# Kernel optimization log

Measured on AMD Instinct MI355X. Metric: run time of the kernel, lower is better.

## Reference

```python
import jax, jax.numpy as jnp
import numpy as np

EMBED_DIM = 1024
NUM_HEADS = 16
HEAD_DIM = EMBED_DIM // NUM_HEADS  # 64
SCALING = 0.125
T, B = 2048, 2


def setup_inputs() -> dict:
    key = jax.random.key(0)
    k_q, k_len, k_w1, k_b1, k_w2, k_b2 = jax.random.split(key, 6)
    query = jax.random.normal(k_q, (T, B, EMBED_DIM), dtype=jnp.float32)
    # realistic padding: each sequence has a valid length in [T//2, T)
    lengths = jax.random.randint(k_len, (B,), T // 2, T)
    key_padding_mask = jnp.arange(T)[None, :] >= lengths[:, None]  # [B, T] bool, True = pad
    s1 = 1.0 / np.sqrt(EMBED_DIM)
    W_in = jax.random.uniform(k_w1, (3 * EMBED_DIM, EMBED_DIM), jnp.float32, -s1, s1)
    b_in = jax.random.uniform(k_b1, (3 * EMBED_DIM,), jnp.float32, -s1, s1)
    W_out = jax.random.uniform(k_w2, (EMBED_DIM, EMBED_DIM), jnp.float32, -s1, s1)
    b_out = jax.random.uniform(k_b2, (EMBED_DIM,), jnp.float32, -s1, s1)
    return {"query": query, "key_padding_mask": key_padding_mask,
            "W_in": W_in, "b_in": b_in, "W_out": W_out, "b_out": b_out}


def reference(query, key_padding_mask, W_in, b_in, W_out, b_out):
    # query: [T, B, E]; key_padding_mask: [B, S] bool (True = padded key)
    t, b, e = query.shape
    h, hd = NUM_HEADS, HEAD_DIM
    proj = query @ W_in.T + b_in                      # [T, B, 3E]
    q, k, v = jnp.split(proj, 3, axis=-1)             # each [T, B, E]
    q = q * SCALING

    def to_bh(x):  # [T, B, E] -> [B*H, T, hd], matching torch view+transpose
        return x.reshape(t, b * h, hd).transpose(1, 0, 2)

    q, k, v = to_bh(q), to_bh(k), to_bh(v)
    attn_weights = jnp.einsum('bth,bsh->bts', q, k)   # [B*H, T, S]
    attn_weights = attn_weights.reshape(b, h, t, t)
    attn_weights = jnp.where(key_padding_mask[:, None, None, :], -jnp.inf, attn_weights)
    # softmax computed in float32 then cast back, as in the original
    attn_weights = jax.nn.softmax(attn_weights.astype(jnp.float32), axis=-1).astype(query.dtype)
    # dropout p=0 (eval/inference) -> identity
    attn = jnp.einsum('bhts,bhsd->bhtd', attn_weights, v.reshape(b, h, t, hd))  # [B,H,T,hd]
    attn = attn.reshape(b * h, t, hd).transpose(1, 0, 2).reshape(t, b, e)       # [T,B,E]
    return attn @ W_out.T + b_out
```

## Files before the change

### kernel.cpp

```cpp
#include <hip/hip_runtime.h>
#include <hip/hip_bf16.h>
#include <stdint.h>
#include <stddef.h>

typedef __hip_bfloat16 bf16;
typedef __attribute__((ext_vector_type(4))) float f32x4;
typedef __attribute__((ext_vector_type(8))) short s16x8;
typedef __attribute__((ext_vector_type(4))) short s16x4;

#define AS1 __attribute__((address_space(1)))
#define AS3 __attribute__((address_space(3)))

__device__ __forceinline__ void async_ld16(const void* g, void* l) {
  __builtin_amdgcn_global_load_lds((AS1 void*)g, (AS3 void*)l, 16, 0, 0);
}

#if __has_builtin(__builtin_amdgcn_exp2f)
#define EXP2F(x) __builtin_amdgcn_exp2f(x)
#else
#define EXP2F(x) exp2f(x)
#endif

__device__ __forceinline__ unsigned pk_bf16(float a, float b) {
  unsigned ua = __builtin_bit_cast(unsigned, a);
  unsigned ub = __builtin_bit_cast(unsigned, b);
  ua += 0x7FFFu + ((ua >> 16) & 1u);
  ub += 0x7FFFu + ((ub >> 16) & 1u);
  return (ua >> 16) | (ub & 0xFFFF0000u);
}

__device__ __forceinline__ unsigned pk_trunc(float a, float b) {
  return __builtin_amdgcn_perm(__builtin_bit_cast(unsigned, b),
                               __builtin_bit_cast(unsigned, a), 0x07060302u);
}

__global__ __launch_bounds__(256) void convert_all_kernel(const float* __restrict__ q_src,
                                                          const float* __restrict__ wi_src,
                                                          const float* __restrict__ wo_src,
                                                          bf16* __restrict__ q_dst,
                                                          bf16* __restrict__ wi_dst,
                                                          bf16* __restrict__ wo_dst,
                                                          const void* __restrict__ mask,
                                                          int* __restrict__ lengths) {
  int blk = blockIdx.x;
  if (blk >= 4096) {
    __shared__ int s_any;
    __shared__ int s_cnt[256];
    const int tid = threadIdx.x;
    const int b = blk - 4096;
    const unsigned char* m8 = (const unsigned char*)mask;
    if (tid == 0) s_any = 0;
    __syncthreads();
    int local = 0;
    for (int i = tid; i < 4096; i += 256) local |= m8[i];
    if (local) atomicOr(&s_any, 1);
    __syncthreads();
    int cnt = 0;
    if (s_any) {
      for (int t = tid; t < 2048; t += 256) cnt += (m8[b * 2048 + t] == 0) ? 1 : 0;
    } else {
      const int* m32 = (const int*)mask;
      for (int t = tid; t < 2048; t += 256) cnt += (m32[b * 2048 + t] == 0) ? 1 : 0;
    }
    s_cnt[tid] = cnt;
    __syncthreads();
    for (int s = 128; s > 0; s >>= 1) {
      if (tid < s) s_cnt[tid] += s_cnt[tid + s];
      __syncthreads();
    }
    if (tid == 0) lengths[b] = s_cnt[0];
    return;
  }
  const float* src;
  bf16* dst;
  int base;
  if (blk < 2048)      { src = q_src;  dst = q_dst;  base = blk * 2048; }
  else if (blk < 3584) { src = wi_src; dst = wi_dst; base = (blk - 2048) * 2048; }
  else                 { src = wo_src; dst = wo_dst; base = (blk - 3584) * 2048; }
  int i = base + threadIdx.x * 8;
  float4 a = *(const float4*)(src + i);
  float4 b = *(const float4*)(src + i + 4);
  unsigned u[4];
  u[0] = pk_bf16(a.x, a.y); u[1] = pk_bf16(a.z, a.w);
  u[2] = pk_bf16(b.x, b.y); u[3] = pk_bf16(b.z, b.w);
  *(uint4*)(dst + i) = *(const uint4*)u;
}

__device__ __forceinline__ void gemm_mainloop(const bf16* __restrict__ A,
                                              const bf16* __restrict__ Bm,
                                              bf16* As, bf16* Bs,
                                              int m0, int n0, f32x4 (&acc)[4][4]) {
  const int K = 1024;
  const int tid = threadIdx.x;
  const int wave = tid >> 6, lane = tid & 63;
  const int col = lane & 15, quad = lane >> 4;
  const int wm = wave & 1, wn = wave >> 1;
#pragma unroll
  for (int mi = 0; mi < 4; mi++)
#pragma unroll
    for (int ni = 0; ni < 4; ni++) acc[mi][ni] = (f32x4){0.f, 0.f, 0.f, 0.f};

  const int c0 = wave * 128 + lane;
  const int rowA0 = c0 >> 2, kc0 = (c0 & 3) * 8;
  const int c1 = c0 + 64;
  const int rowA1 = c1 >> 2, kc1 = (c1 & 3) * 8;
  char* ldsA0 = (char*)As + (size_t)(wave * 128) * 16;
  char* ldsA1 = ldsA0 + 64 * 16;
  char* ldsB0 = (char*)Bs + (size_t)(wave * 128) * 16;
  char* ldsB1 = ldsB0 + 64 * 16;
  const bf16* gA0 = A + (size_t)(m0 + rowA0) * K + kc0;
  const bf16* gA1 = A + (size_t)(m0 + rowA1) * K + kc1;
  const bf16* gB0 = Bm + (size_t)(n0 + rowA0) * K + kc0;
  const bf16* gB1 = Bm + (size_t)(n0 + rowA1) * K + kc1;

  for (int k0 = 0; k0 < K; k0 += 32) {
    async_ld16(gA0 + k0, ldsA0);
    async_ld16(gA1 + k0, ldsA1);
    async_ld16(gB0 + k0, ldsB0);
    async_ld16(gB1 + k0, ldsB1);
    __syncthreads();
    s16x8 af[4], bfr[4];
#pragma unroll
    for (int mi = 0; mi < 4; mi++)
      af[mi] = *(const s16x8*)(As + (wm * 64 + mi * 16 + col) * 32 + quad * 8);
#pragma unroll
    for (int ni = 0; ni < 4; ni++)
      bfr[ni] = *(const s16x8*)(Bs + (wn * 64 + ni * 16 + col) * 32 + quad * 8);
#pragma unroll
    for (int mi = 0; mi < 4; mi++)
#pragma unroll
      for (int ni = 0; ni < 4; ni++)
        acc[mi][ni] = __builtin_amdgcn_mfma_f32_16x16x32_bf16(af[mi], bfr[ni], acc[mi][ni], 0, 0, 0);
    __syncthreads();
  }
}

__global__ __launch_bounds__(256) void gemm_qkv(const bf16* __restrict__ X,
                                                const bf16* __restrict__ W,
                                                const float* __restrict__ bias,
                                                bf16* __restrict__ Qd,
                                                bf16* __restrict__ Kd,
                                                bf16* __restrict__ Vt) {
  __shared__ bf16 As[128 * 32];
  __shared__ bf16 Bs[128 * 32];
  const int m0 = blockIdx.y * 128, n0 = blockIdx.x * 128;
  f32x4 acc[4][4];
  gemm_mainloop(X, W, As, Bs, m0, n0, acc);
  const int tid = threadIdx.x;
  const int wave = tid >> 6, lane = tid & 63;
  const int col = lane & 15, quad = lane >> 4;
  const int wm = wave & 1, wn = wave >> 1;
  const float QSCALE = 0.125f * 1.4426950408889634f;
#pragma unroll
  for (int mi = 0; mi < 4; mi++)
#pragma unroll
    for (int ni = 0; ni < 4; ni++)
#pragma unroll
      for (int r = 0; r < 4; r++) {
        int m = m0 + wm * 64 + mi * 16 + quad * 4 + r;
        int n = n0 + wn * 64 + ni * 16 + col;
        float v = acc[mi][ni][r] + bias[n];
        int e = n & 1023, hh = e >> 6, d = e & 63;
        int t = m >> 1, b = m & 1;
        int bh = b * 16 + hh;
        if (n < 1024) {
          Qd[((size_t)bh * 2048 + t) * 64 + d] = __float2bfloat16(v * QSCALE);
        } else if (n < 2048) {
          Kd[((size_t)bh * 2048 + t) * 64 + d] = __float2bfloat16(v);
        } else {
          int sl = t & 63;
          int perm = ((sl >> 2) & 3) * 16 + (sl >> 4) * 4 + (sl & 3);
          Vt[(size_t)bh * 131072 + (t >> 6) * 4096 + d * 64 + perm] = __float2bfloat16(v);
        }
      }
}

__global__ __launch_bounds__(256, 2) void attn_kernel(const bf16* __restrict__ Qd,
                                                      const bf16* __restrict__ Kd,
                                                      const bf16* __restrict__ Vt,
                                                      const int* __restrict__ lengths,
                                                      bf16* __restrict__ attn_out) {
  __shared__ bf16 Ks[2][64 * 64];
  __shared__ bf16 Vs[2][64 * 64];

  const int bh = blockIdx.y;
  const int b = bh >> 4, h = bh & 15;
  const int qt0 = blockIdx.x * 128;
  const int tid = threadIdx.x;
  const int wave = tid >> 6, lane = tid & 63;
  const int col = lane & 15, quad = lane >> 4;
  const int len = lengths[b];
  const int nfull = len >> 6;
  const int rem = len & 63;
  const int nkt = nfull + (rem ? 1 : 0);

  s16x8 bq[2][2];
#pragma unroll
  for (int g = 0; g < 2; g++) {
    const bf16* qptr =
        Qd + ((size_t)bh * 2048 + qt0 + wave * 32 + g * 16 + col) * 64 + quad * 8;
    bq[g][0] = *(const s16x8*)(qptr);
    bq[g][1] = *(const s16x8*)(qptr + 32);
  }

  const int kbase0 = col * 128 + ((quad ^ (col & 7)) << 4);
  const int kbase1 = kbase0 ^ 64;
  const int vbase0 = col * 128 + (((quad << 1) ^ (col & 7)) << 4);
  const int vbase1 = vbase0 ^ 16;

  const bf16* Kg = Kd + (size_t)bh * 2048 * 64;
  const bf16* Vg = Vt + (size_t)bh * 131072;
  const int c0 = wave * 128 + lane, c1 = c0 + 64;
  const int r0 = c0 >> 3, j0 = (c0 & 7) ^ (r0 & 7);
  const int r1 = c1 >> 3, j1 = (c1 & 7) ^ (r1 & 7);
  const bf16* gK0 = Kg + r0 * 64 + j0 * 8;
  const bf16* gK1 = Kg + r1 * 64 + j1 * 8;
  const bf16* gV0 = Vg + r0 * 64 + j0 * 8;
  const bf16* gV1 = Vg + r1 * 64 + j1 * 8;
  const int dst0 = (wave * 128) * 16, dst1 = (wave * 128 + 64) * 16;

  auto stage = [&](int kt, int BUF) {
    const int off = kt * 4096;
    async_ld16(gK0 + off, (char*)Ks + BUF + dst0);
    async_ld16(gK1 + off, (char*)Ks + BUF + dst1);
    async_ld16(gV0 + off, (char*)Vs + BUF + dst0);
    async_ld16(gV1 + off, (char*)Vs + BUF + dst1);
  };

  const s16x4 aOnes = {0x3F80, 0x3F80, 0x3F80, 0x3F80};
  const f32x4 Zf = (f32x4){0.f, 0.f, 0.f, 0.f};
  f32x4 lacc[2] = {Zf, Zf};
  f32x4 oaccT[2][4];
#pragma unroll
  for (int g = 0; g < 2; g++)
#pragma unroll
    for (int dt = 0; dt < 4; dt++) oaccT[g][dt] = Zf;

  auto score = [&](int BUF, f32x4 (&s0)[4], f32x4 (&s1)[4]) {
#pragma unroll
    for (int ti = 0; ti < 4; ti++) {
      const s16x8 ak0 = *(const s16x8*)((char*)Ks + BUF + ti * 2048 + kbase0);
      s0[ti] = __builtin_amdgcn_mfma_f32_16x16x32_bf16(ak0, bq[0][0], Zf, 0, 0, 0);
      s1[ti] = __builtin_amdgcn_mfma_f32_16x16x32_bf16(ak0, bq[1][0], Zf, 0, 0, 0);
      const s16x8 ak1 = *(const s16x8*)((char*)Ks + BUF + ti * 2048 + kbase1);
      s0[ti] = __builtin_amdgcn_mfma_f32_16x16x32_bf16(ak1, bq[0][1], s0[ti], 0, 0, 0);
      s1[ti] = __builtin_amdgcn_mfma_f32_16x16x32_bf16(ak1, bq[1][1], s1[ti], 0, 0, 0);
    }
  };
  auto accum = [&](int BUF, s16x4 (&bP0)[4], s16x4 (&bP1)[4]) {
#pragma unroll
    for (int ti = 0; ti < 4; ti++) {
      lacc[0] = __builtin_amdgcn_mfma_f32_16x16x16bf16_1k(aOnes, bP0[ti], lacc[0], 0, 0, 0);
      lacc[1] = __builtin_amdgcn_mfma_f32_16x16x16bf16_1k(aOnes, bP1[ti], lacc[1], 0, 0, 0);
    }
#pragma unroll
    for (int dt = 0; dt < 4; dt++) {
#pragma unroll
      for (int sh = 0; sh < 2; sh++) {
        const s16x8 av = *(const s16x8*)((char*)Vs + BUF + dt * 2048 + (sh ? vbase1 : vbase0));
        const s16x4 alo = __builtin_shufflevector(av, av, 0, 1, 2, 3);
        const s16x4 ahi = __builtin_shufflevector(av, av, 4, 5, 6, 7);
        oaccT[0][dt] = __builtin_amdgcn_mfma_f32_16x16x16bf16_1k(alo, bP0[sh * 2], oaccT[0][dt], 0, 0, 0);
        oaccT[0][dt] = __builtin_amdgcn_mfma_f32_16x16x16bf16_1k(ahi, bP0[sh * 2 + 1], oaccT[0][dt], 0, 0, 0);
        oaccT[1][dt] = __builtin_amdgcn_mfma_f32_16x16x16bf16_1k(alo, bP1[sh * 2], oaccT[1][dt], 0, 0, 0);
        oaccT[1][dt] = __builtin_amdgcn_mfma_f32_16x16x16bf16_1k(ahi, bP1[sh * 2 + 1], oaccT[1][dt], 0, 0, 0);
      }
    }
  };

  auto tile_full = [&](int BUF) {
    f32x4 s0[4], s1[4];
    score(BUF, s0, s1);
    s16x4 bP0[4], bP1[4];
#pragma unroll
    for (int ti = 0; ti < 4; ti++) {
      uint2 u0 = {pk_trunc(EXP2F(s0[ti][0]), EXP2F(s0[ti][1])),
                  pk_trunc(EXP2F(s0[ti][2]), EXP2F(s0[ti][3]))};
      bP0[ti] = __builtin_bit_cast(s16x4, u0);
      uint2 u1 = {pk_trunc(EXP2F(s1[ti][0]), EXP2F(s1[ti][1])),
                  pk_trunc(EXP2F(s1[ti][2]), EXP2F(s1[ti][3]))};
      bP1[ti] = __builtin_bit_cast(s16x4, u1);
    }
    accum(BUF, bP0, bP1);
  };

  auto tile_mask = [&](int BUF) {
    f32x4 s0[4], s1[4];
    score(BUF, s0, s1);
    s16x4 bP0[4], bP1[4];
#pragma unroll
    for (int ti = 0; ti < 4; ti++) {
      const int sb = ti * 16 + quad * 4;
      float a0 = (sb + 0 < rem) ? EXP2F(s0[ti][0]) : 0.f;
      float a1 = (sb + 1 < rem) ? EXP2F(s0[ti][1]) : 0.f;
      float a2 = (sb + 2 < rem) ? EXP2F(s0[ti][2]) : 0.f;
      float a3 = (sb + 3 < rem) ? EXP2F(s0[ti][3]) : 0.f;
      uint2 u0 = {pk_trunc(a0, a1), pk_trunc(a2, a3)};
      bP0[ti] = __builtin_bit_cast(s16x4, u0);
      float c0m = (sb + 0 < rem) ? EXP2F(s1[ti][0]) : 0.f;
      float c1m = (sb + 1 < rem) ? EXP2F(s1[ti][1]) : 0.f;
      float c2m = (sb + 2 < rem) ? EXP2F(s1[ti][2]) : 0.f;
      float c3m = (sb + 3 < rem) ? EXP2F(s1[ti][3]) : 0.f;
      uint2 u1 = {pk_trunc(c0m, c1m), pk_trunc(c2m, c3m)};
      bP1[ti] = __builtin_bit_cast(s16x4, u1);
    }
    accum(BUF, bP0, bP1);
  };

  stage(0, 0);
  __syncthreads();
  int kt = 0;
  for (;;) {
    if (kt + 1 < nkt) stage(kt + 1, 8192);
    if (kt < nfull) tile_full(0); else tile_mask(0);
    __syncthreads();
    if (++kt >= nkt) break;
    if (kt + 1 < nkt) stage(kt + 1, 0);
    if (kt < nfull) tile_full(8192); else tile_mask(8192);
    __syncthreads();
    if (++kt >= nkt) break;
  }

#pragma unroll
  for (int g = 0; g < 2; g++) {
    const float linv = 1.0f / lacc[g][0];
    const int t = qt0 + wave * 32 + g * 16 + col;
    bf16* outp = attn_out + ((size_t)t * 2 + b) * 1024 + h * 64 + quad * 4;
#pragma unroll
    for (int dt = 0; dt < 4; dt++) {
      uint2 u = {pk_bf16(oaccT[g][dt][0] * linv, oaccT[g][dt][1] * linv),
                 pk_bf16(oaccT[g][dt][2] * linv, oaccT[g][dt][3] * linv)};
      *(uint2*)(outp + dt * 16) = u;
    }
  }
}

__global__ __launch_bounds__(256) void gemm_out(const bf16* __restrict__ Aa,
                                                const bf16* __restrict__ W,
                                                const float* __restrict__ bias,
                                                float* __restrict__ out) {
  __shared__ bf16 Bs[128 * 64];
  __shared__ bf16 As[64 * 64];
  const int K = 1024;
  const int m0 = blockIdx.y * 64, n0 = blockIdx.x * 128;
  const int tid = threadIdx.x;
  const int wave = tid >> 6, lane = tid & 63;
  const int col = lane & 15, quad = lane >> 4;

  f32x4 acc[8];
#pragma unroll
  for (int ni = 0; ni < 8; ni++) acc[ni] = (f32x4){0.f, 0.f, 0.f, 0.f};

  const bf16* gB[4];
  char* ldsB[4];
#pragma unroll
  for (int i = 0; i < 4; i++) {
    const int c = tid + 256 * i;
    gB[i] = W + (size_t)(n0 + (c >> 3)) * K + (c & 7) * 8;
    ldsB[i] = (char*)Bs + (size_t)(wave * 64 + 256 * i) * 16;
  }
  const bf16* gA[2];
  char* ldsA[2];
#pragma unroll
  for (int i = 0; i < 2; i++) {
    const int c = tid + 256 * i;
    gA[i] = Aa + (size_t)(m0 + (c >> 3)) * K + (c & 7) * 8;
    ldsA[i] = (char*)As + (size_t)(wave * 64 + 256 * i) * 16;
  }

  for (int k0 = 0; k0 < K; k0 += 64) {
#pragma unroll
    for (int i = 0; i < 4; i++) async_ld16(gB[i] + k0, ldsB[i]);
#pragma unroll
    for (int i = 0; i < 2; i++) async_ld16(gA[i] + k0, ldsA[i]);
    __syncthreads();
    const s16x8 af0 = *(const s16x8*)(As + (wave * 16 + col) * 64 + quad * 8);
    const s16x8 af1 = *(const s16x8*)(As + (wave * 16 + col) * 64 + 32 + quad * 8);
#pragma unroll
    for (int ni = 0; ni < 8; ni++) {
      const s16x8 b0 = *(const s16x8*)(Bs + (ni * 16 + col) * 64 + quad * 8);
      acc[ni] = __builtin_amdgcn_mfma_f32_16x16x32_bf16(af0, b0, acc[ni], 0, 0, 0);
      const s16x8 b1 = *(const s16x8*)(Bs + (ni * 16 + col) * 64 + 32 + quad * 8);
      acc[ni] = __builtin_amdgcn_mfma_f32_16x16x32_bf16(af1, b1, acc[ni], 0, 0, 0);
    }
    __syncthreads();
  }

#pragma unroll
  for (int ni = 0; ni < 8; ni++)
#pragma unroll
    for (int r = 0; r < 4; r++) {
      int m = m0 + wave * 16 + quad * 4 + r;
      int n = n0 + ni * 16 + col;
      out[(size_t)m * 1024 + n] = acc[ni][r] + bias[n];
    }
}

extern "C" void kernel_launch(void* const* d_in, const int* in_sizes, int n_in,
                              void* d_out, int out_size, void* d_ws, size_t ws_size,
                              hipStream_t stream) {
  (void)in_sizes; (void)n_in; (void)out_size; (void)ws_size;
  const float* query = (const float*)d_in[0];
  const void*  mask  = d_in[1];
  const float* W_in  = (const float*)d_in[2];
  const float* b_in  = (const float*)d_in[3];
  const float* W_out = (const float*)d_in[4];
  const float* b_out = (const float*)d_in[5];
  float* out = (float*)d_out;

  char* ws = (char*)d_ws;
  bf16* Xbf    = (bf16*)(ws);
  bf16* attnb  = (bf16*)(ws);
  bf16* Winbf  = (bf16*)(ws + 8388608);
  bf16* Woutbf = (bf16*)(ws + 8388608 + 6291456);
  bf16* Qd     = (bf16*)(ws + 16777216);
  bf16* Kd     = (bf16*)(ws + 25165824);
  bf16* Vt     = (bf16*)(ws + 33554432);
  int*  lens   = (int*)(ws + 41943040);

  convert_all_kernel<<<4098, 256, 0, stream>>>(query, W_in, W_out, Xbf, Winbf, Woutbf,
                                               mask, lens);
  gemm_qkv<<<dim3(24, 32), 256, 0, stream>>>(Xbf, Winbf, b_in, Qd, Kd, Vt);
  attn_kernel<<<dim3(16, 32), 256, 0, stream>>>(Qd, Kd, Vt, lens, attnb);
  gemm_out<<<dim3(8, 64), 256, 0, stream>>>(attnb, Woutbf, b_out, out);
}
```

Baseline: 198.0 us.

## Split attention KV range across two wave groups per block and merge in LDS

Each attention block now has 512 threads: two halves of four waves each process the same 128 query rows over disjoint halves of the key tiles. The halves combine their partial output and row-sum accumulators through shared memory before one half writes the result. The grid is also remapped to a 1D index that interleaves batch-heads and query tiles across blocks. The aim is more parallelism per query tile and shorter serial KV loops, in exchange for double the LDS buffers, an extra reduction pass, and lockstep syncs between halves even when their tile counts differ.

```diff
diff --git a/kernel.cpp b/kernel.cpp
--- a/kernel.cpp
+++ b/kernel.cpp
@@ -175,30 +175,37 @@
       }
 }
 
-__global__ __launch_bounds__(256, 2) void attn_kernel(const bf16* __restrict__ Qd,
+__global__ __launch_bounds__(512, 4) void attn_kernel(const bf16* __restrict__ Qd,
                                                       const bf16* __restrict__ Kd,
                                                       const bf16* __restrict__ Vt,
                                                       const int* __restrict__ lengths,
                                                       bf16* __restrict__ attn_out) {
-  __shared__ bf16 Ks[2][64 * 64];
-  __shared__ bf16 Vs[2][64 * 64];
-
-  const int bh = blockIdx.y;
+  __shared__ bf16 Ks[2][2][64 * 64];
+  __shared__ bf16 Vs[2][2][64 * 64];
+
+  const int id = blockIdx.x;
+  const int slot = id >> 3;
+  const int bh = (id & 7) * 4 + (slot & 3);
+  const int qt0 = (slot >> 2) * 128;
   const int b = bh >> 4, h = bh & 15;
-  const int qt0 = blockIdx.x * 128;
+
   const int tid = threadIdx.x;
   const int wave = tid >> 6, lane = tid & 63;
+  const int half = wave >> 2, hw = wave & 3;
   const int col = lane & 15, quad = lane >> 4;
   const int len = lengths[b];
   const int nfull = len >> 6;
   const int rem = len & 63;
   const int nkt = nfull + (rem ? 1 : 0);
+  const int nh0 = (nkt + 1) >> 1;
+  const int first = half ? nh0 : 0;
+  const int cnt = half ? (nkt - nh0) : nh0;
 
   s16x8 bq[2][2];
 #pragma unroll
   for (int g = 0; g < 2; g++) {
     const bf16* qptr =
-        Qd + ((size_t)bh * 2048 + qt0 + wave * 32 + g * 16 + col) * 64 + quad * 8;
+        Qd + ((size_t)bh * 2048 + qt0 + hw * 32 + g * 16 + col) * 64 + quad * 8;
     bq[g][0] = *(const s16x8*)(qptr);
     bq[g][1] = *(const s16x8*)(qptr + 32);
   }
@@ -207,17 +214,18 @@
   const int kbase1 = kbase0 ^ 64;
   const int vbase0 = col * 128 + (((quad << 1) ^ (col & 7)) << 4);
   const int vbase1 = vbase0 ^ 16;
+  const int HBUF = half * 16384;
 
   const bf16* Kg = Kd + (size_t)bh * 2048 * 64;
   const bf16* Vg = Vt + (size_t)bh * 131072;
-  const int c0 = wave * 128 + lane, c1 = c0 + 64;
+  const int c0 = hw * 128 + lane, c1 = c0 + 64;
   const int r0 = c0 >> 3, j0 = (c0 & 7) ^ (r0 & 7);
   const int r1 = c1 >> 3, j1 = (c1 & 7) ^ (r1 & 7);
   const bf16* gK0 = Kg + r0 * 64 + j0 * 8;
   const bf16* gK1 = Kg + r1 * 64 + j1 * 8;
   const bf16* gV0 = Vg + r0 * 64 + j0 * 8;
   const bf16* gV1 = Vg + r1 * 64 + j1 * 8;
-  const int dst0 = (wave * 128) * 16, dst1 = (wave * 128 + 64) * 16;
+  const int dst0 = (hw * 128) * 16, dst1 = (hw * 128 + 64) * 16;
 
   auto stage = [&](int kt, int BUF) {
     const int off = kt * 4096;
@@ -307,30 +315,48 @@
     accum(BUF, bP0, bP1);
   };
 
-  stage(0, 0);
+  stage(first, HBUF);
   __syncthreads();
-  int kt = 0;
-  for (;;) {
-    if (kt + 1 < nkt) stage(kt + 1, 8192);
-    if (kt < nfull) tile_full(0); else tile_mask(0);
-    __syncthreads();
-    if (++kt >= nkt) break;
-    if (kt + 1 < nkt) stage(kt + 1, 0);
-    if (kt < nfull) tile_full(8192); else tile_mask(8192);
-    __syncthreads();
-    if (++kt >= nkt) break;
-  }
-
-#pragma unroll
-  for (int g = 0; g < 2; g++) {
-    const float linv = 1.0f / lacc[g][0];
-    const int t = qt0 + wave * 32 + g * 16 + col;
-    bf16* outp = attn_out + ((size_t)t * 2 + b) * 1024 + h * 64 + quad * 4;
-#pragma unroll
-    for (int dt = 0; dt < 4; dt++) {
-      uint2 u = {pk_bf16(oaccT[g][dt][0] * linv, oaccT[g][dt][1] * linv),
-                 pk_bf16(oaccT[g][dt][2] * linv, oaccT[g][dt][3] * linv)};
-      *(uint2*)(outp + dt * 16) = u;
+  for (int i = 0; i < nh0; i++) {
+    if (i + 1 < cnt) stage(first + i + 1, HBUF + ((i + 1) & 1) * 8192);
+    if (i < cnt) {
+      const int kt = first + i;
+      const int BUF = HBUF + (i & 1) * 8192;
+      if (kt < nfull) tile_full(BUF); else tile_mask(BUF);
+    }
+    __syncthreads();
+  }
+
+  float* OF = (float*)Ks;
+  float* LF = (float*)Vs;
+  const int me = hw * 64 + lane;
+  if (half == 1) {
+#pragma unroll
+    for (int g = 0; g < 2; g++) {
+      LF[g * 256 + me] = lacc[g][0];
+#pragma unroll
+      for (int dt = 0; dt < 4; dt++)
+#pragma unroll
+        for (int r = 0; r < 4; r++)
+          OF[(g * 16 + dt * 4 + r) * 256 + me] = oaccT[g][dt][r];
+    }
+  }
+  __syncthreads();
+  if (half == 0) {
+#pragma unroll
+    for (int g = 0; g < 2; g++) {
+      const float linv = 1.0f / (lacc[g][0] + LF[g * 256 + me]);
+      const int t = qt0 + hw * 32 + g * 16 + col;
+      bf16* outp = attn_out + ((size_t)t * 2 + b) * 1024 + h * 64 + quad * 4;
+#pragma unroll
+      for (int dt = 0; dt < 4; dt++) {
+        float o0 = (oaccT[g][dt][0] + OF[(g * 16 + dt * 4 + 0) * 256 + me]) * linv;
+        float o1 = (oaccT[g][dt][1] + OF[(g * 16 + dt * 4 + 1) * 256 + me]) * linv;
+        float o2 = (oaccT[g][dt][2] + OF[(g * 16 + dt * 4 + 2) * 256 + me]) * linv;
+        float o3 = (oaccT[g][dt][3] + OF[(g * 16 + dt * 4 + 3) * 256 + me]) * linv;
+        uint2 u = {pk_bf16(o0, o1), pk_bf16(o2, o3)};
+        *(uint2*)(outp + dt * 16) = u;
+      }
     }
   }
 }
@@ -421,6 +447,6 @@
   convert_all_kernel<<<4098, 256, 0, stream>>>(query, W_in, W_out, Xbf, Winbf, Woutbf,
                                                mask, lens);
   gemm_qkv<<<dim3(24, 32), 256, 0, stream>>>(Xbf, Winbf, b_in, Qd, Kd, Vt);
-  attn_kernel<<<dim3(16, 32), 256, 0, stream>>>(Qd, Kd, Vt, lens, attnb);
+  attn_kernel<<<512, 512, 0, stream>>>(Qd, Kd, Vt, lens, attnb);
   gemm_out<<<dim3(8, 64), 256, 0, stream>>>(attnb, Woutbf, b_out, out);
 }
```

After: 196.0 us. Within noise of the previous version (-1.0%).
